# Performance work log

Hardware: AMD Instinct MI355X
Metric: run time of the kernel (lower is better)

The kernel has to match this reference:

```python
import jax, jax.numpy as jnp
import numpy as np

N = 100000   # nodes
E = 1600000  # edges (avg degree 16)
D = 64       # in_channels
OUT = 64     # out_channels


def setup_inputs() -> dict:
    key = jax.random.key(0)
    k1, k2, k3, k4, k5 = jax.random.split(key, 5)
    x = jax.random.normal(k1, (N, D), jnp.float32)
    edge_index = jax.random.randint(k2, (2, E), 0, N, dtype=jnp.int32)
    x0 = jax.random.normal(k3, (N, D), jnp.float32)
    W_weight = jax.random.normal(k4, (OUT, D), jnp.float32) * (1.0 / np.sqrt(D))
    W_bias = jax.random.normal(k5, (OUT,), jnp.float32) * 0.01
    return {"x": x, "edge_index": edge_index, "x0": x0,
            "W_weight": W_weight, "W_bias": W_bias}


def reference(x, edge_index, x0, W_bias, W_weight):
    n = x.shape[0]
    # gcn_norm with add_self_loops=True (PyG default), improved=False
    self_loops = jnp.arange(n, dtype=edge_index.dtype)
    row = jnp.concatenate([edge_index[0], self_loops])  # source nodes
    col = jnp.concatenate([edge_index[1], self_loops])  # target nodes
    w = jnp.ones(row.shape[0], dtype=x.dtype)
    deg = jax.ops.segment_sum(w, col, num_segments=n)   # in-degree (+1 self loop)
    deg_inv_sqrt = jnp.where(deg > 0, jax.lax.rsqrt(jnp.maximum(deg, 1e-12)), 0.0)
    norm = deg_inv_sqrt[row] * deg_inv_sqrt[col]        # [E+N]
    # SpMM: adj_t = SparseTensor(row=col, col=row) -> out[c] = sum_e norm_e * x[row_e]
    agg = jax.ops.segment_sum(x[row] * norm[:, None], col, num_segments=n)  # [N, D]
    # use_init=False, use_weight=True -> trailing Linear
    return agg @ W_weight.T + W_bias
```

## Files before the change

kernel.cpp:

```cpp
#include <hip/hip_runtime.h>


#define NBMAX 400
#define CAP   5120

typedef short bf16x8 __attribute__((ext_vector_type(8)));
typedef float f32x4  __attribute__((ext_vector_type(4)));

__device__ inline float bflo(unsigned u) { return __uint_as_float(u << 16); }
__device__ inline float bfhi(unsigned u) { return __uint_as_float(u & 0xFFFF0000u); }
__device__ inline unsigned short f2bf(float f) {
    unsigned u = __float_as_uint(f);
    u += 0x7FFFu + ((u >> 16) & 1u);
    return (unsigned short)(u >> 16);
}

__global__ __launch_bounds__(512) void k_bin(const int* __restrict__ row,
                                             const int* __restrict__ col,
                                             int* __restrict__ gcnt,
                                             unsigned int* __restrict__ ebuf, int E) {
    __shared__ unsigned int   sorted4[4096];
    __shared__ unsigned short sbkt[4096];
    __shared__ int h[NBMAX], hstart[NBMAX], hcur[NBMAX], gof[NBMAX];
    int t = threadIdx.x;
    int base = blockIdx.x * 4096;
    int total = min(4096, E - base);

    int rr[8], cc[8];
    #pragma unroll
    for (int i = 0; i < 2; ++i) {
        int e0 = (t + i * 512) * 4;
        if (e0 + 3 < total) {
            int4 r4 = *(const int4*)(row + base + e0);
            int4 c4 = *(const int4*)(col + base + e0);
            rr[i*4+0]=r4.x; rr[i*4+1]=r4.y; rr[i*4+2]=r4.z; rr[i*4+3]=r4.w;
            cc[i*4+0]=c4.x; cc[i*4+1]=c4.y; cc[i*4+2]=c4.z; cc[i*4+3]=c4.w;
        } else {
            #pragma unroll
            for (int j = 0; j < 4; ++j) {
                int e = e0 + j;
                if (e < total) { rr[i*4+j] = row[base+e]; cc[i*4+j] = col[base+e]; }
                else cc[i*4+j] = -1;
            }
        }
    }
    for (int b = t; b < NBMAX; b += 512) h[b] = 0;
    __syncthreads();
    #pragma unroll
    for (int i = 0; i < 8; ++i)
        if (cc[i] >= 0) atomicAdd(&h[cc[i] >> 8], 1);
    __syncthreads();
    if (t < 64) {
        int lo = t * 7;
        int loc[7]; int s = 0;
        #pragma unroll
        for (int i = 0; i < 7; ++i) {
            loc[i] = s;
            int idx = lo + i;
            s += (idx < NBMAX) ? h[idx] : 0;
        }
        int incl = s;
        for (int off = 1; off < 64; off <<= 1) {
            int v = __shfl_up(incl, off);
            if (t >= off) incl += v;
        }
        int ex = incl - s;
        #pragma unroll
        for (int i = 0; i < 7; ++i) {
            int idx = lo + i;
            if (idx < NBMAX) hstart[idx] = ex + loc[i];
        }
    }
    __syncthreads();
    for (int b = t; b < NBMAX; b += 512) hcur[b] = hstart[b];
    __syncthreads();
    #pragma unroll
    for (int i = 0; i < 8; ++i) {
        if (cc[i] >= 0) {
            int b = cc[i] >> 8;
            int rank = atomicAdd(&hcur[b], 1);
            sorted4[rank] = (unsigned)rr[i] | ((unsigned)(cc[i] & 255) << 24);
            sbkt[rank] = (unsigned short)b;
        }
    }
    for (int b = t; b < NBMAX; b += 512) {
        int m = h[b];
        gof[b] = b * CAP + (m ? atomicAdd(&gcnt[b], m) : 0);
    }
    __syncthreads();
    for (int i = t; i < total; i += 512) {
        int b = sbkt[i];
        ebuf[gof[b] + (i - hstart[b])] = sorted4[i];
    }
}

__global__ __launch_bounds__(512) void k_gemmcnt(const float* __restrict__ x,
                                                 const float* __restrict__ W,
                                                 const unsigned int* __restrict__ ebuf,
                                                 const int* __restrict__ gcnt,
                                                 unsigned short* __restrict__ yb, int n) {
    __shared__ __align__(16) unsigned short xs[128][72];
    __shared__ __align__(16) unsigned short Wb[64][72];
    __shared__ int hd[128];
    int t = threadIdx.x;
    long long total = (long long)n * 64;
    long long xbase = (long long)blockIdx.x * 8192;
    if (t < 128) hd[t] = 0;
    #pragma unroll
    for (int i = 0; i < 4; ++i) {
        int idx = t + i * 512;
        int r = idx >> 4, c4 = (idx & 15) << 2;
        long long g = xbase + (long long)idx * 4;
        float4 v;
        if (g + 3 < total) v = *(const float4*)(x + g);
        else {
            v.x = (g + 0 < total) ? x[g + 0] : 0.f;
            v.y = (g + 1 < total) ? x[g + 1] : 0.f;
            v.z = (g + 2 < total) ? x[g + 2] : 0.f;
            v.w = (g + 3 < total) ? x[g + 3] : 0.f;
        }
        ushort4 o; o.x = f2bf(v.x); o.y = f2bf(v.y); o.z = f2bf(v.z); o.w = f2bf(v.w);
        *(ushort4*)&xs[r][c4] = o;
    }
    #pragma unroll
    for (int i = 0; i < 2; ++i) {
        int idx = t + i * 512;
        int r = idx >> 4, c4 = (idx & 15) << 2;
        float4 wv = *(const float4*)(W + idx * 4);
        ushort4 wo; wo.x = f2bf(wv.x); wo.y = f2bf(wv.y); wo.z = f2bf(wv.z); wo.w = f2bf(wv.w);
        *(ushort4*)&Wb[r][c4] = wo;
    }
    {
        int bb  = blockIdx.x >> 1;
        int sub = blockIdx.x & 1;
        int s0 = bb * CAP;
        int count = min(gcnt[bb], CAP);
        for (int i = t; i < count; i += 512) {
            unsigned d = ebuf[s0 + i] >> 24;
            if ((int)(d >> 7) == sub) atomicAdd(&hd[d & 127], 1);
        }
    }
    __syncthreads();
    int lane = t & 63, wid = t >> 6;
    int m  = wid * 16 + (lane & 15);
    int kg = (lane >> 4) * 8;
    bf16x8 a0 = *(bf16x8*)&xs[m][kg];
    bf16x8 a1 = *(bf16x8*)&xs[m][32 + kg];
    int bn = lane & 15;
    f32x4 acc0 = {0.f,0.f,0.f,0.f}, acc1 = acc0, acc2 = acc0, acc3 = acc0;
    {
        bf16x8 b0 = *(bf16x8*)&Wb[bn][kg], b1 = *(bf16x8*)&Wb[bn][32 + kg];
        acc0 = __builtin_amdgcn_mfma_f32_16x16x32_bf16(a0, b0, acc0, 0, 0, 0);
        acc0 = __builtin_amdgcn_mfma_f32_16x16x32_bf16(a1, b1, acc0, 0, 0, 0);
    }
    {
        bf16x8 b0 = *(bf16x8*)&Wb[bn + 16][kg], b1 = *(bf16x8*)&Wb[bn + 16][32 + kg];
        acc1 = __builtin_amdgcn_mfma_f32_16x16x32_bf16(a0, b0, acc1, 0, 0, 0);
        acc1 = __builtin_amdgcn_mfma_f32_16x16x32_bf16(a1, b1, acc1, 0, 0, 0);
    }
    {
        bf16x8 b0 = *(bf16x8*)&Wb[bn + 32][kg], b1 = *(bf16x8*)&Wb[bn + 32][32 + kg];
        acc2 = __builtin_amdgcn_mfma_f32_16x16x32_bf16(a0, b0, acc2, 0, 0, 0);
        acc2 = __builtin_amdgcn_mfma_f32_16x16x32_bf16(a1, b1, acc2, 0, 0, 0);
    }
    {
        bf16x8 b0 = *(bf16x8*)&Wb[bn + 48][kg], b1 = *(bf16x8*)&Wb[bn + 48][32 + kg];
        acc3 = __builtin_amdgcn_mfma_f32_16x16x32_bf16(a0, b0, acc3, 0, 0, 0);
        acc3 = __builtin_amdgcn_mfma_f32_16x16x32_bf16(a1, b1, acc3, 0, 0, 0);
    }
    int lr0 = wid * 16 + (lane >> 4) * 4;
    int rbase = blockIdx.x * 128 + lr0;
    #pragma unroll
    for (int i = 0; i < 4; ++i) {
        int r = rbase + i;
        if (r < n) {
            float dv = rsqrtf((float)hd[lr0 + i] + 1.0f);
            long long ro = (long long)r * 64 + bn;
            yb[ro +  0] = f2bf(dv * acc0[i]);
            yb[ro + 16] = f2bf(dv * acc1[i]);
            yb[ro + 32] = f2bf(dv * acc2[i]);
            yb[ro + 48] = f2bf(dv * acc3[i]);
        }
    }
}

__global__ __launch_bounds__(1024) void k_aggr(const unsigned int* __restrict__ ebuf,
                                               const int* __restrict__ gcnt,
                                               const unsigned short* __restrict__ yb,
                                               const float* __restrict__ bias,
                                               float* __restrict__ out, int n) {
    __shared__ int h[256], hstart[256], hc[256], wsum[4];
    __shared__ int sbuf[CAP];
    int b = blockIdx.x, t = threadIdx.x;
    int s0 = b * CAP;
    int count = min(gcnt[b], CAP);

    if (t < 256) h[t] = 0;
    __syncthreads();
    unsigned rec[5];
    #pragma unroll
    for (int k = 0; k < 5; ++k) {
        int i = t + k * 1024;
        if (i < count) {
            unsigned p = ebuf[s0 + i];
            rec[k] = p;
            atomicAdd(&h[p >> 24], 1);
        }
    }
    __syncthreads();
    if (t < 256) {
        int v = h[t];
        int lane = t & 63, wid = t >> 6;
        int incl = v;
        #pragma unroll
        for (int off = 1; off < 64; off <<= 1) {
            int u = __shfl_up(incl, off);
            if (lane >= off) incl += u;
        }
        hstart[t] = incl;
        if (lane == 63) wsum[wid] = incl;
    }
    __syncthreads();
    if (t < 256) {
        int wid = t >> 6;
        int add = 0;
        for (int w = 0; w < wid; ++w) add += wsum[w];
        int ex = hstart[t] - h[t] + add;
        hstart[t] = ex;
        hc[t] = ex;
    }
    __syncthreads();
    #pragma unroll
    for (int k = 0; k < 5; ++k) {
        int i = t + k * 1024;
        if (i < count) {
            unsigned p = rec[k];
            int r = atomicAdd(&hc[p >> 24], 1);
            sbuf[r] = (int)(p & 0x1FFFFu);
        }
    }
    __syncthreads();

    int lane = t & 63, w = t >> 6;
    int g = lane >> 4, q = lane & 15;
    #pragma unroll
    for (int r = 0; r < 4; ++r) {
        int cl = r * 64 + w * 4 + g;
        int c = b * 256 + cl;
        if (c >= n) continue;
        int start = hstart[cl], len = h[cl];
        float a0 = 0.f, a1 = 0.f, a2 = 0.f, a3 = 0.f;
        if (len > 0) {
            int sc = sbuf[start];
            for (int i = 0; i < len; ++i) {
                int sn = (i + 1 < len) ? sbuf[start + i + 1] : 0;
                float2 v = *(const float2*)(yb + (long long)sc * 64 + (q << 2));
                unsigned u0 = __float_as_uint(v.x), u1 = __float_as_uint(v.y);
                a0 += bflo(u0); a1 += bfhi(u0);
                a2 += bflo(u1); a3 += bfhi(u1);
                sc = sn;
            }
        }
        {
            float2 v = *(const float2*)(yb + (long long)c * 64 + (q << 2));
            unsigned u0 = __float_as_uint(v.x), u1 = __float_as_uint(v.y);
            a0 += bflo(u0); a1 += bfhi(u0);
            a2 += bflo(u1); a3 += bfhi(u1);
        }
        float dc = rsqrtf((float)len + 1.0f);
        float4 bv = *(const float4*)(bias + (q << 2));
        *(float4*)(out + (long long)c * 64 + (q << 2)) =
            make_float4(dc * a0 + bv.x, dc * a1 + bv.y,
                        dc * a2 + bv.z, dc * a3 + bv.w);
    }
}

extern "C" void kernel_launch(void* const* d_in, const int* in_sizes, int n_in,
                              void* d_out, int out_size, void* d_ws, size_t ws_size,
                              hipStream_t stream) {
    const float* x    = (const float*)d_in[0];
    const int*   ei   = (const int*)d_in[1];
    const float* W    = (const float*)d_in[3];
    const float* bias = (const float*)d_in[4];
    float* out = (float*)d_out;

    int n = in_sizes[0] / 64;
    int E = in_sizes[1] / 2;
    const int* row = ei;
    const int* col = ei + E;

    int NB = (n + 255) / 256;

    char* ws = (char*)d_ws;
    size_t off = 0;
    auto alloc = [&](size_t bytes) { char* p = ws + off; off += (bytes + 15) & ~size_t(15); return p; };
    int*            gcnt = (int*)  alloc((size_t)NB * 4);
    unsigned short* yb   = (unsigned short*)alloc((size_t)n * 64 * 2);
    unsigned int*   ebuf = (unsigned int*)alloc((size_t)NB * CAP * 4);

    int nbE = (E + 4095) / 4096;

    hipMemsetAsync(gcnt, 0, (size_t)NB * 4, stream);
    k_bin    <<<nbE, 512, 0, stream>>>(row, col, gcnt, ebuf, E);
    k_gemmcnt<<<(n + 127) / 128, 512, 0, stream>>>(x, W, ebuf, gcnt, yb, n);
    k_aggr   <<<NB, 1024, 0, stream>>>(ebuf, gcnt, yb, bias, out, n);
}
```

Measured before the change: 173.5 us.

## Fuse bin, GEMM and aggregation into one cooperative persistent kernel

Replaces the memset plus three kernel launches with a single cooperative-launch kernel that uses grid syncs between phases: edge binning, per-block bf16 MFMA transform of 256 rows, degree count and scaling into yb, then per-bucket local sort and gather aggregation. It aims to remove launch gaps and the extra passes over ebuf. In exchange it pays for grid-wide barriers, runs aggregation at 512 threads with a serialized per-node loop, and falls back to the old path if cooperative launch is unavailable. Zeroing gcnt inside the kernel relies on the first grid sync happening before any atomics on gcnt.

```diff
diff --git a/kernel.cpp b/kernel.cpp
--- a/kernel.cpp
+++ b/kernel.cpp
@@ -1,4 +1,7 @@
 #include <hip/hip_runtime.h>
+#include <hip/hip_cooperative_groups.h>
+
+namespace cg = cooperative_groups;
 
 
 #define NBMAX 400
@@ -15,15 +18,34 @@
     return (unsigned short)(u >> 16);
 }
 
-__global__ __launch_bounds__(512) void k_bin(const int* __restrict__ row,
-                                             const int* __restrict__ col,
-                                             int* __restrict__ gcnt,
-                                             unsigned int* __restrict__ ebuf, int E) {
-    __shared__ unsigned int   sorted4[4096];
-    __shared__ unsigned short sbkt[4096];
-    __shared__ int h[NBMAX], hstart[NBMAX], hcur[NBMAX], gof[NBMAX];
-    int t = threadIdx.x;
-    int base = blockIdx.x * 4096;
+#define MFMA __builtin_amdgcn_mfma_f32_16x16x32_bf16
+
+__global__ __launch_bounds__(512, 4) void k_mega(
+    const int* __restrict__ row, const int* __restrict__ col,
+    const float* __restrict__ x, const float* __restrict__ W,
+    const float* __restrict__ bias,
+    int* __restrict__ gcnt, unsigned int* __restrict__ ebuf,
+    unsigned short* __restrict__ yb, float* __restrict__ out,
+    int E, int n, int NB)
+{
+    __shared__ __align__(16) char smem[32000];
+    int*  hd = (int*)smem;
+    char* ph = smem + 1024;
+
+    cg::grid_group gg = cg::this_grid();
+    int bx = blockIdx.x, t = threadIdx.x;
+    int lane = t & 63, wid = t >> 6;
+
+    if (t == 0 && bx < NB) gcnt[bx] = 0;
+
+    unsigned int*   sorted4 = (unsigned int*)ph;
+    unsigned short* sbkt    = (unsigned short*)(ph + 16384);
+    int* h      = (int*)(ph + 24576);
+    int* hstart = (int*)(ph + 26176);
+    int* hcur   = (int*)(ph + 27776);
+    int* gof    = (int*)(ph + 29376);
+
+    int base  = bx * 4096;
     int total = min(4096, E - base);
 
     int rr[8], cc[8];
@@ -83,6 +105,270 @@
             sbkt[rank] = (unsigned short)b;
         }
     }
+    __threadfence();
+    gg.sync();
+
+    for (int b = t; b < NBMAX; b += 512) {
+        int m = h[b];
+        gof[b] = b * CAP + (m ? atomicAdd(&gcnt[b], m) : 0);
+    }
+    __syncthreads();
+    for (int i = t; i < total; i += 512) {
+        int b = sbkt[i];
+        ebuf[gof[b] + (i - hstart[b])] = sorted4[i];
+    }
+    __syncthreads();
+
+    unsigned short (*xs)[72] = (unsigned short (*)[72])ph;
+    unsigned short (*Wb)[72] = (unsigned short (*)[72])(ph + 18432);
+    long long tot64 = (long long)n * 64;
+
+    #pragma unroll
+    for (int i = 0; i < 2; ++i) {
+        int idx = t + i * 512;
+        int r = idx >> 4, c4 = (idx & 15) << 2;
+        float4 wv = *(const float4*)(W + idx * 4);
+        ushort4 wo; wo.x = f2bf(wv.x); wo.y = f2bf(wv.y); wo.z = f2bf(wv.z); wo.w = f2bf(wv.w);
+        *(ushort4*)&Wb[r][c4] = wo;
+    }
+    int mrow = wid * 16 + (lane & 15);
+    int kg   = (lane >> 4) * 8;
+    int bn   = lane & 15;
+    f32x4 A0 = {0.f,0.f,0.f,0.f}, A1 = A0, A2 = A0, A3 = A0;
+    f32x4 B0 = A0, B1 = A0, B2 = A0, B3 = A0;
+
+    {
+        long long xb = (long long)bx * 16384;
+        #pragma unroll
+        for (int i = 0; i < 4; ++i) {
+            int idx = t + i * 512;
+            int r = idx >> 4, c4 = (idx & 15) << 2;
+            long long g = xb + (long long)idx * 4;
+            float4 v;
+            if (g + 3 < tot64) v = *(const float4*)(x + g);
+            else {
+                v.x = (g + 0 < tot64) ? x[g + 0] : 0.f;
+                v.y = (g + 1 < tot64) ? x[g + 1] : 0.f;
+                v.z = (g + 2 < tot64) ? x[g + 2] : 0.f;
+                v.w = (g + 3 < tot64) ? x[g + 3] : 0.f;
+            }
+            ushort4 o; o.x = f2bf(v.x); o.y = f2bf(v.y); o.z = f2bf(v.z); o.w = f2bf(v.w);
+            *(ushort4*)&xs[r][c4] = o;
+        }
+        __syncthreads();
+        bf16x8 a0 = *(bf16x8*)&xs[mrow][kg];
+        bf16x8 a1 = *(bf16x8*)&xs[mrow][32 + kg];
+        { bf16x8 b0 = *(bf16x8*)&Wb[bn     ][kg], b1 = *(bf16x8*)&Wb[bn     ][32+kg];
+          A0 = MFMA(a0,b0,A0,0,0,0); A0 = MFMA(a1,b1,A0,0,0,0); }
+        { bf16x8 b0 = *(bf16x8*)&Wb[bn + 16][kg], b1 = *(bf16x8*)&Wb[bn + 16][32+kg];
+          A1 = MFMA(a0,b0,A1,0,0,0); A1 = MFMA(a1,b1,A1,0,0,0); }
+        { bf16x8 b0 = *(bf16x8*)&Wb[bn + 32][kg], b1 = *(bf16x8*)&Wb[bn + 32][32+kg];
+          A2 = MFMA(a0,b0,A2,0,0,0); A2 = MFMA(a1,b1,A2,0,0,0); }
+        { bf16x8 b0 = *(bf16x8*)&Wb[bn + 48][kg], b1 = *(bf16x8*)&Wb[bn + 48][32+kg];
+          A3 = MFMA(a0,b0,A3,0,0,0); A3 = MFMA(a1,b1,A3,0,0,0); }
+        __syncthreads();
+    }
+    {
+        long long xb = (long long)bx * 16384 + 8192;
+        #pragma unroll
+        for (int i = 0; i < 4; ++i) {
+            int idx = t + i * 512;
+            int r = idx >> 4, c4 = (idx & 15) << 2;
+            long long g = xb + (long long)idx * 4;
+            float4 v;
+            if (g + 3 < tot64) v = *(const float4*)(x + g);
+            else {
+                v.x = (g + 0 < tot64) ? x[g + 0] : 0.f;
+                v.y = (g + 1 < tot64) ? x[g + 1] : 0.f;
+                v.z = (g + 2 < tot64) ? x[g + 2] : 0.f;
+                v.w = (g + 3 < tot64) ? x[g + 3] : 0.f;
+            }
+            ushort4 o; o.x = f2bf(v.x); o.y = f2bf(v.y); o.z = f2bf(v.z); o.w = f2bf(v.w);
+            *(ushort4*)&xs[r][c4] = o;
+        }
+        __syncthreads();
+        bf16x8 a0 = *(bf16x8*)&xs[mrow][kg];
+        bf16x8 a1 = *(bf16x8*)&xs[mrow][32 + kg];
+        { bf16x8 b0 = *(bf16x8*)&Wb[bn     ][kg], b1 = *(bf16x8*)&Wb[bn     ][32+kg];
+          B0 = MFMA(a0,b0,B0,0,0,0); B0 = MFMA(a1,b1,B0,0,0,0); }
+        { bf16x8 b0 = *(bf16x8*)&Wb[bn + 16][kg], b1 = *(bf16x8*)&Wb[bn + 16][32+kg];
+          B1 = MFMA(a0,b0,B1,0,0,0); B1 = MFMA(a1,b1,B1,0,0,0); }
+        { bf16x8 b0 = *(bf16x8*)&Wb[bn + 32][kg], b1 = *(bf16x8*)&Wb[bn + 32][32+kg];
+          B2 = MFMA(a0,b0,B2,0,0,0); B2 = MFMA(a1,b1,B2,0,0,0); }
+        { bf16x8 b0 = *(bf16x8*)&Wb[bn + 48][kg], b1 = *(bf16x8*)&Wb[bn + 48][32+kg];
+          B3 = MFMA(a0,b0,B3,0,0,0); B3 = MFMA(a1,b1,B3,0,0,0); }
+    }
+    __threadfence();
+    gg.sync();
+
+    if (t < 256) hd[t] = 0;
+    __syncthreads();
+    int s0  = bx * CAP;
+    int cnt = (bx < NB) ? min(gcnt[bx], CAP) : 0;
+    for (int i = t; i < cnt; i += 512) atomicAdd(&hd[ebuf[s0 + i] >> 24], 1);
+    __syncthreads();
+    {
+        int lr0 = wid * 16 + (lane >> 4) * 4;
+        #pragma unroll
+        for (int i = 0; i < 4; ++i) {
+            int lr = lr0 + i;
+            int r  = bx * 256 + lr;
+            if (r < n) {
+                float dv = rsqrtf((float)hd[lr] + 1.0f);
+                long long ro = (long long)r * 64 + bn;
+                yb[ro +  0] = f2bf(dv * A0[i]);
+                yb[ro + 16] = f2bf(dv * A1[i]);
+                yb[ro + 32] = f2bf(dv * A2[i]);
+                yb[ro + 48] = f2bf(dv * A3[i]);
+            }
+            int r2 = r + 128, lr2 = lr + 128;
+            if (r2 < n) {
+                float dv = rsqrtf((float)hd[lr2] + 1.0f);
+                long long ro = (long long)r2 * 64 + bn;
+                yb[ro +  0] = f2bf(dv * B0[i]);
+                yb[ro + 16] = f2bf(dv * B1[i]);
+                yb[ro + 32] = f2bf(dv * B2[i]);
+                yb[ro + 48] = f2bf(dv * B3[i]);
+            }
+        }
+    }
+    __threadfence();
+    gg.sync();
+
+    int* ahstart = (int*)ph;
+    int* ahc     = (int*)(ph + 1024);
+    int* awsum   = (int*)(ph + 2048);
+    int* sbuf    = (int*)(ph + 2112);
+    if (t < 256) {
+        int v = hd[t];
+        int l = t & 63, w4 = t >> 6;
+        int incl = v;
+        #pragma unroll
+        for (int off = 1; off < 64; off <<= 1) {
+            int u = __shfl_up(incl, off);
+            if (l >= off) incl += u;
+        }
+        ahstart[t] = incl;
+        if (l == 63) awsum[w4] = incl;
+    }
+    __syncthreads();
+    if (t < 256) {
+        int w4 = t >> 6;
+        int add = 0;
+        for (int w = 0; w < w4; ++w) add += awsum[w];
+        int ex = ahstart[t] - hd[t] + add;
+        ahstart[t] = ex;
+        ahc[t] = ex;
+    }
+    __syncthreads();
+    for (int i = t; i < cnt; i += 512) {
+        unsigned p = ebuf[s0 + i];
+        int rk = atomicAdd(&ahc[p >> 24], 1);
+        sbuf[rk] = (int)(p & 0x1FFFFu);
+    }
+    __syncthreads();
+
+    int g = lane >> 4, q = lane & 15;
+    #pragma unroll 1
+    for (int r = 0; r < 8; ++r) {
+        int cl = r * 32 + wid * 4 + g;
+        int c = bx * 256 + cl;
+        if (c >= n) continue;
+        int start = ahstart[cl], len = hd[cl];
+        float a0 = 0.f, a1 = 0.f, a2 = 0.f, a3 = 0.f;
+        if (len > 0) {
+            int sc = sbuf[start];
+            for (int i = 0; i < len; ++i) {
+                int sn = (i + 1 < len) ? sbuf[start + i + 1] : 0;
+                float2 v = *(const float2*)(yb + (long long)sc * 64 + (q << 2));
+                unsigned u0 = __float_as_uint(v.x), u1 = __float_as_uint(v.y);
+                a0 += bflo(u0); a1 += bfhi(u0);
+                a2 += bflo(u1); a3 += bfhi(u1);
+                sc = sn;
+            }
+        }
+        {
+            float2 v = *(const float2*)(yb + (long long)c * 64 + (q << 2));
+            unsigned u0 = __float_as_uint(v.x), u1 = __float_as_uint(v.y);
+            a0 += bflo(u0); a1 += bfhi(u0);
+            a2 += bflo(u1); a3 += bfhi(u1);
+        }
+        float dc = rsqrtf((float)len + 1.0f);
+        float4 bv = *(const float4*)(bias + (q << 2));
+        *(float4*)(out + (long long)c * 64 + (q << 2)) =
+            make_float4(dc * a0 + bv.x, dc * a1 + bv.y,
+                        dc * a2 + bv.z, dc * a3 + bv.w);
+    }
+}
+
+__global__ __launch_bounds__(512) void k_bin(const int* __restrict__ row,
+                                             const int* __restrict__ col,
+                                             int* __restrict__ gcnt,
+                                             unsigned int* __restrict__ ebuf, int E) {
+    __shared__ unsigned int   sorted4[4096];
+    __shared__ unsigned short sbkt[4096];
+    __shared__ int h[NBMAX], hstart[NBMAX], hcur[NBMAX], gof[NBMAX];
+    int t = threadIdx.x;
+    int base = blockIdx.x * 4096;
+    int total = min(4096, E - base);
+
+    int rr[8], cc[8];
+    #pragma unroll
+    for (int i = 0; i < 2; ++i) {
+        int e0 = (t + i * 512) * 4;
+        if (e0 + 3 < total) {
+            int4 r4 = *(const int4*)(row + base + e0);
+            int4 c4 = *(const int4*)(col + base + e0);
+            rr[i*4+0]=r4.x; rr[i*4+1]=r4.y; rr[i*4+2]=r4.z; rr[i*4+3]=r4.w;
+            cc[i*4+0]=c4.x; cc[i*4+1]=c4.y; cc[i*4+2]=c4.z; cc[i*4+3]=c4.w;
+        } else {
+            #pragma unroll
+            for (int j = 0; j < 4; ++j) {
+                int e = e0 + j;
+                if (e < total) { rr[i*4+j] = row[base+e]; cc[i*4+j] = col[base+e]; }
+                else cc[i*4+j] = -1;
+            }
+        }
+    }
+    for (int b = t; b < NBMAX; b += 512) h[b] = 0;
+    __syncthreads();
+    #pragma unroll
+    for (int i = 0; i < 8; ++i)
+        if (cc[i] >= 0) atomicAdd(&h[cc[i] >> 8], 1);
+    __syncthreads();
+    if (t < 64) {
+        int lo = t * 7;
+        int loc[7]; int s = 0;
+        #pragma unroll
+        for (int i = 0; i < 7; ++i) {
+            loc[i] = s;
+            int idx = lo + i;
+            s += (idx < NBMAX) ? h[idx] : 0;
+        }
+        int incl = s;
+        for (int off = 1; off < 64; off <<= 1) {
+            int v = __shfl_up(incl, off);
+            if (t >= off) incl += v;
+        }
+        int ex = incl - s;
+        #pragma unroll
+        for (int i = 0; i < 7; ++i) {
+            int idx = lo + i;
+            if (idx < NBMAX) hstart[idx] = ex + loc[i];
+        }
+    }
+    __syncthreads();
+    for (int b = t; b < NBMAX; b += 512) hcur[b] = hstart[b];
+    __syncthreads();
+    #pragma unroll
+    for (int i = 0; i < 8; ++i) {
+        if (cc[i] >= 0) {
+            int b = cc[i] >> 8;
+            int rank = atomicAdd(&hcur[b], 1);
+            sorted4[rank] = (unsigned)rr[i] | ((unsigned)(cc[i] & 255) << 24);
+            sbkt[rank] = (unsigned short)b;
+        }
+    }
     for (int b = t; b < NBMAX; b += 512) {
         int m = h[b];
         gof[b] = b * CAP + (m ? atomicAdd(&gcnt[b], m) : 0);
@@ -150,23 +436,23 @@
     f32x4 acc0 = {0.f,0.f,0.f,0.f}, acc1 = acc0, acc2 = acc0, acc3 = acc0;
     {
         bf16x8 b0 = *(bf16x8*)&Wb[bn][kg], b1 = *(bf16x8*)&Wb[bn][32 + kg];
-        acc0 = __builtin_amdgcn_mfma_f32_16x16x32_bf16(a0, b0, acc0, 0, 0, 0);
-        acc0 = __builtin_amdgcn_mfma_f32_16x16x32_bf16(a1, b1, acc0, 0, 0, 0);
+        acc0 = MFMA(a0, b0, acc0, 0, 0, 0);
+        acc0 = MFMA(a1, b1, acc0, 0, 0, 0);
     }
     {
         bf16x8 b0 = *(bf16x8*)&Wb[bn + 16][kg], b1 = *(bf16x8*)&Wb[bn + 16][32 + kg];
-        acc1 = __builtin_amdgcn_mfma_f32_16x16x32_bf16(a0, b0, acc1, 0, 0, 0);
-        acc1 = __builtin_amdgcn_mfma_f32_16x16x32_bf16(a1, b1, acc1, 0, 0, 0);
+        acc1 = MFMA(a0, b0, acc1, 0, 0, 0);
+        acc1 = MFMA(a1, b1, acc1, 0, 0, 0);
     }
     {
         bf16x8 b0 = *(bf16x8*)&Wb[bn + 32][kg], b1 = *(bf16x8*)&Wb[bn + 32][32 + kg];
-        acc2 = __builtin_amdgcn_mfma_f32_16x16x32_bf16(a0, b0, acc2, 0, 0, 0);
-        acc2 = __builtin_amdgcn_mfma_f32_16x16x32_bf16(a1, b1, acc2, 0, 0, 0);
+        acc2 = MFMA(a0, b0, acc2, 0, 0, 0);
+        acc2 = MFMA(a1, b1, acc2, 0, 0, 0);
     }
     {
         bf16x8 b0 = *(bf16x8*)&Wb[bn + 48][kg], b1 = *(bf16x8*)&Wb[bn + 48][32 + kg];
-        acc3 = __builtin_amdgcn_mfma_f32_16x16x32_bf16(a0, b0, acc3, 0, 0, 0);
-        acc3 = __builtin_amdgcn_mfma_f32_16x16x32_bf16(a1, b1, acc3, 0, 0, 0);
+        acc3 = MFMA(a0, b0, acc3, 0, 0, 0);
+        acc3 = MFMA(a1, b1, acc3, 0, 0, 0);
     }
     int lr0 = wid * 16 + (lane >> 4) * 4;
     int rbase = blockIdx.x * 128 + lr0;
@@ -298,10 +584,28 @@
     unsigned short* yb   = (unsigned short*)alloc((size_t)n * 64 * 2);
     unsigned int*   ebuf = (unsigned int*)alloc((size_t)NB * CAP * 4);
 
-    int nbE = (E + 4095) / 4096;
-
-    hipMemsetAsync(gcnt, 0, (size_t)NB * 4, stream);
-    k_bin    <<<nbE, 512, 0, stream>>>(row, col, gcnt, ebuf, E);
-    k_gemmcnt<<<(n + 127) / 128, 512, 0, stream>>>(x, W, ebuf, gcnt, yb, n);
-    k_aggr   <<<NB, 1024, 0, stream>>>(ebuf, gcnt, yb, bias, out, n);
+    int nbE  = (E + 4095) / 4096;
+    int grid = (nbE > NB) ? nbE : NB;
+
+    bool coop = false;
+    int dev = 0;
+    if (hipGetDevice(&dev) == hipSuccess) {
+        int attr = 0, ncu = 0, maxblk = 0;
+        hipDeviceGetAttribute(&attr, hipDeviceAttributeCooperativeLaunch, dev);
+        hipDeviceGetAttribute(&ncu, hipDeviceAttributeMultiprocessorCount, dev);
+        hipError_t e = hipOccupancyMaxActiveBlocksPerMultiprocessor(&maxblk, k_mega, 512, 0);
+        if (attr && ncu > 0 && e == hipSuccess && (long long)maxblk * ncu >= grid) coop = true;
+    }
+
+    if (coop) {
+        void* args[] = {(void*)&row, (void*)&col, (void*)&x, (void*)&W, (void*)&bias,
+                        (void*)&gcnt, (void*)&ebuf, (void*)&yb, (void*)&out,
+                        (void*)&E, (void*)&n, (void*)&NB};
+        hipLaunchCooperativeKernel((void*)k_mega, dim3(grid), dim3(512), args, 0, stream);
+    } else {
+        hipMemsetAsync(gcnt, 0, (size_t)NB * 4, stream);
+        k_bin    <<<nbE, 512, 0, stream>>>(row, col, gcnt, ebuf, E);
+        k_gemmcnt<<<(n + 127) / 128, 512, 0, stream>>>(x, W, ebuf, gcnt, yb, n);
+        k_aggr   <<<NB, 1024, 0, stream>>>(ebuf, gcnt, yb, bias, out, n);
+    }
 }
```

After: 505.4 us. 2.91x slower.
